# Kernel optimization log

Measured on AMD Instinct MI355X. Metric: run time of the kernel, lower is better.

Reference implementation:

```python
import jax, jax.numpy as jnp
import numpy as np

N_NODES = 100_000
N_EDGES = 1_600_000
F_IN = 32
F_OUT = 32
DIM = 2
K = 5                      # kernel_size per dim (open spline)
KTOT = K ** DIM            # 25 kernel weight matrices
S = 2 ** DIM               # 4 nonzero linear-B-spline basis terms per edge
NEG_SLOPE = 0.2

# offsets over the 2^DIM corners of the spline cell, [S, DIM]
_OFFSETS = np.array([[(s >> d) & 1 for d in range(DIM)] for s in range(S)], dtype=np.int32)
_STRIDES = np.array([K ** d for d in range(DIM)], dtype=np.int32)


def _spline_basis(pseudo):
    """Degree-1 open B-spline basis. pseudo: [E, DIM] in [0,1].
    Returns basis [E, S] and kernel-weight indices widx [E, S]."""
    offsets = jnp.asarray(_OFFSETS)
    strides = jnp.asarray(_STRIDES)
    p = pseudo * (K - 1)                         # open spline scaling
    fl = jnp.floor(p)
    frac = p - fl                                # [E, DIM]
    b = jnp.where(offsets[None] == 0, 1.0 - frac[:, None, :], frac[:, None, :])
    basis = jnp.prod(b, axis=-1)                 # [E, S]
    idx = jnp.clip(fl.astype(jnp.int32)[:, None, :] + offsets[None], 0, K - 1)
    widx = jnp.sum(idx * strides, axis=-1)       # [E, S] in [0, KTOT)
    return basis, widx


def setup_inputs() -> dict:
    key = jax.random.key(0)
    ks = jax.random.split(key, 7)
    x = jax.random.normal(ks[0], (N_NODES, F_IN), dtype=jnp.float32)
    edge_index = jax.random.randint(ks[1], (2, N_EDGES), 0, N_NODES)
    pseudo = jax.random.uniform(ks[2], (N_EDGES, DIM), dtype=jnp.float32)
    bound = 1.0 / np.sqrt(KTOT * F_IN)           # matches reset_parameters uniform(size, ...)
    weight = jax.random.uniform(ks[3], (KTOT, F_IN, F_OUT), jnp.float32, -bound, bound)
    root_weight = jax.random.uniform(ks[4], (F_IN, F_OUT), jnp.float32, -bound, bound)
    att_weight = jax.random.uniform(ks[5], (2 * F_OUT,), jnp.float32, -bound, bound)
    bias = jax.random.uniform(ks[6], (F_OUT,), jnp.float32, -bound, bound)
    return {"x": x, "edge_index": edge_index, "pseudo": pseudo, "weight": weight,
            "root_weight": root_weight, "att_weight": att_weight, "bias": bias}


def reference(x, edge_index, pseudo, weight, root_weight, att_weight, bias):
    row, col = edge_index[0], edge_index[1]      # row = target, col = source
    basis, widx = _spline_basis(pseudo)          # [E,S], [E,S]

    # Precompute x @ W_k for every kernel weight: [N, KTOT, F_OUT]
    xw = jnp.einsum('nf,kfo->nko', x, weight)
    flat = col[:, None] * KTOT + widx            # [E, S] flat (node, kernel) index
    gathered = xw.reshape(-1, F_OUT)[flat]       # [E, S, F_OUT]
    msg = jnp.einsum('es,esf->ef', basis, gathered)  # spline-weighted edge messages

    x_root = x @ root_weight                     # [N, F_OUT]

    # GAT-style attention logits: cat([x_root[row], msg]) . att_weight
    alpha = x_root[row] @ att_weight[:F_OUT] + msg @ att_weight[F_OUT:]
    alpha = jnp.where(alpha > 0, alpha, NEG_SLOPE * alpha)  # leaky relu

    # segment softmax over incoming edges of each target node
    amax = jax.ops.segment_max(alpha, row, num_segments=N_NODES)
    amax = jnp.where(jnp.isfinite(amax), amax, 0.0)
    ex = jnp.exp(alpha - amax[row])
    denom = jax.ops.segment_sum(ex, row, num_segments=N_NODES)
    att = ex / (denom[row] + 1e-16)

    out = jax.ops.segment_sum(msg * att[:, None], row, num_segments=N_NODES)
    return out + x_root + bias
```

## Files before the change

### kernel.cpp

```cpp
#include <hip/hip_runtime.h>
#include <stdint.h>

#define N_NODES 100000
#define N_EDGES 1600000
#define NBLK_SCAN 391

typedef __attribute__((ext_vector_type(8))) short short8;
typedef __attribute__((ext_vector_type(4))) float float4v;

__device__ __forceinline__ unsigned short f32_to_bf16(float f) {
  uint32_t u = __float_as_uint(f);
  u += 0x7fffu + ((u >> 16) & 1u);
  return (unsigned short)(u >> 16);
}
__device__ __forceinline__ float bf16_to_f32(unsigned short h) {
  return __uint_as_float(((uint32_t)h) << 16);
}

__global__ __launch_bounds__(256) void k_zero(
    const float* __restrict__ weight, const float* __restrict__ root_w,
    int* __restrict__ deg, unsigned short* __restrict__ wbf) {
  int tid = threadIdx.x;
  int b = blockIdx.x;
  int i = b * 256 + tid;
  if (i < N_NODES) deg[i] = 0;
  if (b < 100) {
    int e = i;
    int t = e >> 9, rem = e & 511;
    int q = rem >> 7, row = (rem >> 3) & 15, j = rem & 7;
    int km = t >> 1, fin = q * 8 + j, fo = (t & 1) * 16 + row;
    wbf[e] = f32_to_bf16(weight[(km * 32 + fin) * 32 + fo]);
  } else if (b == 100) {
    for (int idx = tid; idx < 1024; idx += 256) {
      int t = 50 + (idx >> 9), rem = idx & 511;
      int q = rem >> 7, row = (rem >> 3) & 15, j = rem & 7;
      int fin = q * 8 + j, fo = (t - 50) * 16 + row;
      wbf[t * 512 + rem] = f32_to_bf16(root_w[fin * 32 + fo]);
    }
  }
}

__global__ __launch_bounds__(256) void k1_xw(
    const float* __restrict__ x, const unsigned short* __restrict__ wbf,
    const int* __restrict__ ei, const float* __restrict__ att_w,
    const float* __restrict__ bias,
    int* __restrict__ deg, unsigned short* __restrict__ rank,
    unsigned short* __restrict__ xw, float* __restrict__ out,
    uint2* __restrict__ od) {
  __shared__ __align__(16) uint2 st[3200];
  int tid = threadIdx.x;
  int b = blockIdx.x;

  int e = b * 256 + tid;
  int rk = atomicAdd(&deg[ei[e]], 1);

  int wave = tid >> 6, lane = tid & 63;
  int quad = lane >> 4, c16 = lane & 15;
  int n0 = b * 16;
  int node = n0 + c16;
  const float* xp = x + (size_t)node * 32 + quad * 8;
  float4 a0 = *reinterpret_cast<const float4*>(xp);
  float4 a1 = *reinterpret_cast<const float4*>(xp + 4);
  short8 af;
  af[0] = (short)f32_to_bf16(a0.x); af[1] = (short)f32_to_bf16(a0.y);
  af[2] = (short)f32_to_bf16(a0.z); af[3] = (short)f32_to_bf16(a0.w);
  af[4] = (short)f32_to_bf16(a1.x); af[5] = (short)f32_to_bf16(a1.y);
  af[6] = (short)f32_to_bf16(a1.z); af[7] = (short)f32_to_bf16(a1.w);

  float rsum = 0.f;
  for (int idx = 0; idx < 13; idx++) {
    int t = wave * 13 + idx;
    short8 bf = *reinterpret_cast<const short8*>(wbf + ((t * 4 + quad) * 16 + c16) * 8);
    float4v acc = {0.f, 0.f, 0.f, 0.f};
    acc = __builtin_amdgcn_mfma_f32_16x16x32_bf16(bf, af, acc, 0, 0, 0);
    if (t < 50) {
      uint2 pk;
      pk.x = (unsigned int)f32_to_bf16(acc[0]) |
             ((unsigned int)f32_to_bf16(acc[1]) << 16);
      pk.y = (unsigned int)f32_to_bf16(acc[2]) |
             ((unsigned int)f32_to_bf16(acc[3]) << 16);
      int tq = t * 4 + quad;
      st[tq * 16 + (c16 ^ (tq & 15))] = pk;
    } else {
      int gfo = (t - 50) * 16 + quad * 4;
      float4 bi = *reinterpret_cast<const float4*>(bias + gfo);
      float4 o;
      o.x = acc[0] + bi.x; o.y = acc[1] + bi.y;
      o.z = acc[2] + bi.z; o.w = acc[3] + bi.w;
      *reinterpret_cast<float4*>(out + (size_t)node * 32 + gfo) = o;
      float4 aw = *reinterpret_cast<const float4*>(att_w + gfo);
      rsum += acc[0] * aw.x + acc[1] * aw.y + acc[2] * aw.z + acc[3] * aw.w;
    }
  }
  if (wave == 3) {
    rsum += __shfl_xor(rsum, 16);
    rsum += __shfl_xor(rsum, 32);
    if (lane < 16) od[node].y = __float_as_uint(rsum);
  }
  __syncthreads();
  uint2* dst = reinterpret_cast<uint2*>(xw) + (size_t)n0 * 200;
  for (int j = tid; j < 3200; j += 256) {
    int nd = j / 200;
    int tq = j - nd * 200;
    dst[j] = st[tq * 16 + (nd ^ (tq & 15))];
  }
  rank[e] = (unsigned short)rk;
}

__global__ __launch_bounds__(256) void kscan1(const int* __restrict__ deg,
                                              int* __restrict__ incl,
                                              int* __restrict__ bsum) {
  __shared__ int s[256];
  int tid = threadIdx.x;
  int i = blockIdx.x * 256 + tid;
  int v = (i < N_NODES) ? deg[i] : 0;
  s[tid] = v;
  __syncthreads();
  for (int d = 1; d < 256; d <<= 1) {
    int t = (tid >= d) ? s[tid - d] : 0;
    __syncthreads();
    s[tid] += t;
    __syncthreads();
  }
  if (i < N_NODES) incl[i] = s[tid];
  if (tid == 255) bsum[blockIdx.x] = s[255];
}

__global__ __launch_bounds__(512) void kscan2(const int* __restrict__ bsum,
                                              int* __restrict__ bbase) {
  __shared__ int s[512];
  int tid = threadIdx.x;
  int v = (tid < NBLK_SCAN) ? bsum[tid] : 0;
  s[tid] = v;
  __syncthreads();
  for (int d = 1; d < 512; d <<= 1) {
    int t = (tid >= d) ? s[tid - d] : 0;
    __syncthreads();
    s[tid] += t;
    __syncthreads();
  }
  if (tid < NBLK_SCAN) bbase[tid] = s[tid] - v;
}

__global__ __launch_bounds__(256) void kscan3(const int* __restrict__ deg,
                                              int* __restrict__ offs,
                                              const int* __restrict__ bbase,
                                              uint2* __restrict__ od) {
  int i = blockIdx.x * 256 + threadIdx.x;
  if (i < N_NODES) {
    int v = offs[i] - deg[i] + bbase[i >> 8];
    offs[i] = v;
    od[i].x = (unsigned int)v;
  }
  if (i == 0) {
    offs[N_NODES] = N_EDGES;
    od[N_NODES].x = (unsigned int)N_EDGES;
  }
}

__global__ __launch_bounds__(256) void kscatter(
    const int* __restrict__ ei, const float* __restrict__ pseudo,
    const uint2* __restrict__ od, const unsigned short* __restrict__ rank,
    uint2* __restrict__ epack) {
  int e = blockIdx.x * 256 + threadIdx.x;
  int r = ei[e];
  int c = ei[N_EDGES + e];
  float p0 = pseudo[2 * e] * 4.f;
  float p1 = pseudo[2 * e + 1] * 4.f;
  int rk = rank[e];
  unsigned int offr = od[r].x;
  float fl0 = floorf(p0), fl1 = floorf(p1);
  float fr0 = p0 - fl0, fr1 = p1 - fl1;
  int i0 = (int)fl0, i1 = (int)fl1;
  int w0 = i0 + 5 * i1;
  int w2 = w0 + 5;
  unsigned int q0 = (unsigned int)(fr0 * 65535.f + 0.5f);
  unsigned int q1 = (unsigned int)(fr1 * 65535.f + 0.5f);
  uint2 pk;
  pk.x = (unsigned int)c | ((unsigned int)w0 << 17) | ((unsigned int)w2 << 22);
  pk.y = q0 | (q1 << 16);
  epack[offr + rk] = pk;
}

__global__ __launch_bounds__(256) void k2_csr(
    const uint2* __restrict__ od, const uint2* __restrict__ epack,
    const unsigned short* __restrict__ xw, const float* __restrict__ att_w,
    float* __restrict__ out) {
  int tid = threadIdx.x;
  int wave = tid >> 6, lane = tid & 63;
  int node = blockIdx.x * 4 + wave;
  if (node >= N_NODES) return;
  int f = lane & 31, half = lane >> 5;
  uint2 v0 = od[node];
  int s0 = (int)v0.x;
  int s1 = (int)od[node + 1].x;
  float rd = __uint_as_float(v0.y);
  float a2 = att_w[32 + f];
  const unsigned short* xwf = xw + f;
  float acc = 0.f, den = 0.f;
  int i = s0 + half;
  const float Q = 1.f / 65535.f;

  for (; i + 6 < s1; i += 8) {
    uint2 p[4];
    p[0] = epack[i];     p[1] = epack[i + 2];
    p[2] = epack[i + 4]; p[3] = epack[i + 6];
    int col[4], o0[4], o2[4];
    float fr0[4], fr1[4];
#pragma unroll
    for (int u = 0; u < 4; u++) {
      col[u] = (int)(p[u].x & 0x1FFFF);
      o0[u] = (int)((p[u].x >> 17) & 31) * 32;
      o2[u] = (int)((p[u].x >> 22) & 31) * 32;
      fr0[u] = (float)(p[u].y & 0xffff) * Q;
      fr1[u] = (float)(p[u].y >> 16) * Q;
    }
    float g0[4], g1[4], g2[4], g3[4];
#pragma unroll
    for (int u = 0; u < 4; u++) {
      const unsigned short* base = xwf + (size_t)col[u] * 800;
      g0[u] = bf16_to_f32(base[o0[u]]);
      g1[u] = bf16_to_f32(base[o0[u] + 32]);
      g2[u] = bf16_to_f32(base[o2[u]]);
      g3[u] = bf16_to_f32(base[o2[u] + 32]);
    }
    float msg[4], t[4];
#pragma unroll
    for (int u = 0; u < 4; u++) {
      float c0 = 1.f - fr0[u], c1 = 1.f - fr1[u];
      msg[u] = c1 * (c0 * g0[u] + fr0[u] * g1[u]) +
               fr1[u] * (c0 * g2[u] + fr0[u] * g3[u]);
      t[u] = msg[u] * a2;
    }
#pragma unroll
    for (int m = 16; m >= 1; m >>= 1) {
      t[0] += __shfl_xor(t[0], m);
      t[1] += __shfl_xor(t[1], m);
      t[2] += __shfl_xor(t[2], m);
      t[3] += __shfl_xor(t[3], m);
    }
#pragma unroll
    for (int u = 0; u < 4; u++) {
      float alpha = rd + t[u];
      alpha = alpha > 0.f ? alpha : 0.2f * alpha;
      float ex = __expf(alpha);
      acc += msg[u] * ex;
      den += ex;
    }
  }
  for (; i < s1; i += 2) {
    uint2 pv = epack[i];
    int col = (int)(pv.x & 0x1FFFF);
    int o0 = (int)((pv.x >> 17) & 31) * 32;
    int o2 = (int)((pv.x >> 22) & 31) * 32;
    float fr0 = (float)(pv.y & 0xffff) * Q;
    float fr1 = (float)(pv.y >> 16) * Q;
    const unsigned short* base = xwf + (size_t)col * 800;
    float g0 = bf16_to_f32(base[o0]);
    float g1 = bf16_to_f32(base[o0 + 32]);
    float g2 = bf16_to_f32(base[o2]);
    float g3 = bf16_to_f32(base[o2 + 32]);
    float c0 = 1.f - fr0, c1 = 1.f - fr1;
    float msg = c1 * (c0 * g0 + fr0 * g1) + fr1 * (c0 * g2 + fr0 * g3);
    float t = msg * a2;
#pragma unroll
    for (int m = 16; m >= 1; m >>= 1) t += __shfl_xor(t, m);
    float alpha = rd + t;
    alpha = alpha > 0.f ? alpha : 0.2f * alpha;
    float ex = __expf(alpha);
    acc += msg * ex;
    den += ex;
  }

  acc += __shfl_xor(acc, 32);
  den += __shfl_xor(den, 32);
  if (half == 0) out[node * 32 + f] += acc / (den + 1e-16f);
}

extern "C" void kernel_launch(void* const* d_in, const int* in_sizes, int n_in,
                              void* d_out, int out_size, void* d_ws, size_t ws_size,
                              hipStream_t stream) {
  const float* x      = (const float*)d_in[0];
  const int*   ei     = (const int*)d_in[1];
  const float* pseudo = (const float*)d_in[2];
  const float* weight = (const float*)d_in[3];
  const float* root_w = (const float*)d_in[4];
  const float* att_w  = (const float*)d_in[5];
  const float* bias   = (const float*)d_in[6];
  float* out = (float*)d_out;

  char* ws = (char*)d_ws;
  unsigned short* xw   = (unsigned short*)ws;
  uint2* od            = (uint2*)(ws + 160000000);
  unsigned short* wbf  = (unsigned short*)(ws + 160800016);
  int* deg             = (int*)(ws + 160853264);
  int* offs            = (int*)(ws + 161253264);
  int* bsum            = (int*)(ws + 161653280);
  int* bbase           = (int*)(ws + 161654880);
  unsigned short* rank = (unsigned short*)(ws + 161656480);
  uint2* epack         = (uint2*)(ws + 164856480);

  hipLaunchKernelGGL(k_zero, dim3(NBLK_SCAN), dim3(256), 0, stream,
                     weight, root_w, deg, wbf);
  hipLaunchKernelGGL(k1_xw, dim3(6250), dim3(256), 0, stream,
                     x, wbf, ei, att_w, bias, deg, rank, xw, out, od);
  hipLaunchKernelGGL(kscan1, dim3(NBLK_SCAN), dim3(256), 0, stream, deg, offs, bsum);
  hipLaunchKernelGGL(kscan2, dim3(1), dim3(512), 0, stream, bsum, bbase);
  hipLaunchKernelGGL(kscan3, dim3(NBLK_SCAN), dim3(256), 0, stream, deg, offs, bbase, od);
  hipLaunchKernelGGL(kscatter, dim3(6250), dim3(256), 0, stream,
                     ei, pseudo, od, rank, epack);
  hipLaunchKernelGGL(k2_csr, dim3(25000), dim3(256), 0, stream,
                     od, epack, xw, att_w, out);
}
```

Before: 333.0 us.

## Replace rank array with atomic cursor scatter and precompute xw offsets

The per-edge rank from the degree-count atomic is no longer stored. The CSR scatter now takes its slot with an atomicAdd on a per-node cursor that the scan initialises. The packed edge word now holds the full xw element offset (col*800 + w0*32), so the aggregation kernel does no bit unpacking and uses fixed strides for the four corner loads. The xw tile store uses nontemporal stores. Edge order within a row becomes nondeterministic, which changes floating-point summation order, and the scatter now pays for a second round of atomics.

```diff
diff --git a/kernel.cpp b/kernel.cpp
--- a/kernel.cpp
+++ b/kernel.cpp
@@ -44,7 +44,7 @@
     const float* __restrict__ x, const unsigned short* __restrict__ wbf,
     const int* __restrict__ ei, const float* __restrict__ att_w,
     const float* __restrict__ bias,
-    int* __restrict__ deg, unsigned short* __restrict__ rank,
+    int* __restrict__ deg,
     unsigned short* __restrict__ xw, float* __restrict__ out,
     uint2* __restrict__ od) {
   __shared__ __align__(16) uint2 st[3200];
@@ -52,7 +52,7 @@
   int b = blockIdx.x;
 
   int e = b * 256 + tid;
-  int rk = atomicAdd(&deg[ei[e]], 1);
+  atomicAdd(&deg[ei[e]], 1);
 
   int wave = tid >> 6, lane = tid & 63;
   int quad = lane >> 4, c16 = lane & 15;
@@ -98,13 +98,15 @@
     if (lane < 16) od[node].y = __float_as_uint(rsum);
   }
   __syncthreads();
-  uint2* dst = reinterpret_cast<uint2*>(xw) + (size_t)n0 * 200;
+  unsigned long long* dst =
+      reinterpret_cast<unsigned long long*>(xw) + (size_t)n0 * 200;
+  const unsigned long long* stq =
+      reinterpret_cast<const unsigned long long*>(st);
   for (int j = tid; j < 3200; j += 256) {
     int nd = j / 200;
     int tq = j - nd * 200;
-    dst[j] = st[tq * 16 + (nd ^ (tq & 15))];
-  }
-  rank[e] = (unsigned short)rk;
+    __builtin_nontemporal_store(stq[tq * 16 + (nd ^ (tq & 15))], dst + j);
+  }
 }
 
 __global__ __launch_bounds__(256) void kscan1(const int* __restrict__ deg,
@@ -143,43 +145,38 @@
 }
 
 __global__ __launch_bounds__(256) void kscan3(const int* __restrict__ deg,
-                                              int* __restrict__ offs,
+                                              const int* __restrict__ incl,
                                               const int* __restrict__ bbase,
-                                              uint2* __restrict__ od) {
+                                              uint2* __restrict__ od,
+                                              int* __restrict__ cur) {
   int i = blockIdx.x * 256 + threadIdx.x;
   if (i < N_NODES) {
-    int v = offs[i] - deg[i] + bbase[i >> 8];
-    offs[i] = v;
+    int v = incl[i] - deg[i] + bbase[i >> 8];
     od[i].x = (unsigned int)v;
-  }
-  if (i == 0) {
-    offs[N_NODES] = N_EDGES;
-    od[N_NODES].x = (unsigned int)N_EDGES;
-  }
+    cur[i] = v;
+  }
+  if (i == 0) od[N_NODES].x = (unsigned int)N_EDGES;
 }
 
 __global__ __launch_bounds__(256) void kscatter(
     const int* __restrict__ ei, const float* __restrict__ pseudo,
-    const uint2* __restrict__ od, const unsigned short* __restrict__ rank,
-    uint2* __restrict__ epack) {
+    int* __restrict__ cur, uint2* __restrict__ epack) {
   int e = blockIdx.x * 256 + threadIdx.x;
   int r = ei[e];
   int c = ei[N_EDGES + e];
   float p0 = pseudo[2 * e] * 4.f;
   float p1 = pseudo[2 * e + 1] * 4.f;
-  int rk = rank[e];
-  unsigned int offr = od[r].x;
   float fl0 = floorf(p0), fl1 = floorf(p1);
   float fr0 = p0 - fl0, fr1 = p1 - fl1;
   int i0 = (int)fl0, i1 = (int)fl1;
   int w0 = i0 + 5 * i1;
-  int w2 = w0 + 5;
   unsigned int q0 = (unsigned int)(fr0 * 65535.f + 0.5f);
   unsigned int q1 = (unsigned int)(fr1 * 65535.f + 0.5f);
+  int pos = atomicAdd(&cur[r], 1);
   uint2 pk;
-  pk.x = (unsigned int)c | ((unsigned int)w0 << 17) | ((unsigned int)w2 << 22);
+  pk.x = (unsigned int)(c * 800 + w0 * 32);
   pk.y = q0 | (q1 << 16);
-  epack[offr + rk] = pk;
+  epack[pos] = pk;
 }
 
 __global__ __launch_bounds__(256) void k2_csr(
@@ -205,24 +202,20 @@
     uint2 p[4];
     p[0] = epack[i];     p[1] = epack[i + 2];
     p[2] = epack[i + 4]; p[3] = epack[i + 6];
-    int col[4], o0[4], o2[4];
     float fr0[4], fr1[4];
 #pragma unroll
     for (int u = 0; u < 4; u++) {
-      col[u] = (int)(p[u].x & 0x1FFFF);
-      o0[u] = (int)((p[u].x >> 17) & 31) * 32;
-      o2[u] = (int)((p[u].x >> 22) & 31) * 32;
       fr0[u] = (float)(p[u].y & 0xffff) * Q;
       fr1[u] = (float)(p[u].y >> 16) * Q;
     }
     float g0[4], g1[4], g2[4], g3[4];
 #pragma unroll
     for (int u = 0; u < 4; u++) {
-      const unsigned short* base = xwf + (size_t)col[u] * 800;
-      g0[u] = bf16_to_f32(base[o0[u]]);
-      g1[u] = bf16_to_f32(base[o0[u] + 32]);
-      g2[u] = bf16_to_f32(base[o2[u]]);
-      g3[u] = bf16_to_f32(base[o2[u] + 32]);
+      const unsigned short* base = xwf + p[u].x;
+      g0[u] = bf16_to_f32(base[0]);
+      g1[u] = bf16_to_f32(base[32]);
+      g2[u] = bf16_to_f32(base[160]);
+      g3[u] = bf16_to_f32(base[192]);
     }
     float msg[4], t[4];
 #pragma unroll
@@ -250,16 +243,13 @@
   }
   for (; i < s1; i += 2) {
     uint2 pv = epack[i];
-    int col = (int)(pv.x & 0x1FFFF);
-    int o0 = (int)((pv.x >> 17) & 31) * 32;
-    int o2 = (int)((pv.x >> 22) & 31) * 32;
     float fr0 = (float)(pv.y & 0xffff) * Q;
     float fr1 = (float)(pv.y >> 16) * Q;
-    const unsigned short* base = xwf + (size_t)col * 800;
-    float g0 = bf16_to_f32(base[o0]);
-    float g1 = bf16_to_f32(base[o0 + 32]);
-    float g2 = bf16_to_f32(base[o2]);
-    float g3 = bf16_to_f32(base[o2 + 32]);
+    const unsigned short* base = xwf + pv.x;
+    float g0 = bf16_to_f32(base[0]);
+    float g1 = bf16_to_f32(base[32]);
+    float g2 = bf16_to_f32(base[160]);
+    float g3 = bf16_to_f32(base[192]);
     float c0 = 1.f - fr0, c1 = 1.f - fr1;
     float msg = c1 * (c0 * g0 + fr0 * g1) + fr1 * (c0 * g2 + fr0 * g3);
     float t = msg * a2;
@@ -294,21 +284,22 @@
   uint2* od            = (uint2*)(ws + 160000000);
   unsigned short* wbf  = (unsigned short*)(ws + 160800016);
   int* deg             = (int*)(ws + 160853264);
-  int* offs            = (int*)(ws + 161253264);
-  int* bsum            = (int*)(ws + 161653280);
-  int* bbase           = (int*)(ws + 161654880);
-  unsigned short* rank = (unsigned short*)(ws + 161656480);
-  uint2* epack         = (uint2*)(ws + 164856480);
+  int* incl            = (int*)(ws + 161253264);
+  int* cur             = (int*)(ws + 161653264);
+  int* bsum            = (int*)(ws + 162053264);
+  int* bbase           = (int*)(ws + 162054864);
+  uint2* epack         = (uint2*)(ws + 162056464);
 
   hipLaunchKernelGGL(k_zero, dim3(NBLK_SCAN), dim3(256), 0, stream,
                      weight, root_w, deg, wbf);
   hipLaunchKernelGGL(k1_xw, dim3(6250), dim3(256), 0, stream,
-                     x, wbf, ei, att_w, bias, deg, rank, xw, out, od);
-  hipLaunchKernelGGL(kscan1, dim3(NBLK_SCAN), dim3(256), 0, stream, deg, offs, bsum);
+                     x, wbf, ei, att_w, bias, deg, xw, out, od);
+  hipLaunchKernelGGL(kscan1, dim3(NBLK_SCAN), dim3(256), 0, stream, deg, incl, bsum);
   hipLaunchKernelGGL(kscan2, dim3(1), dim3(512), 0, stream, bsum, bbase);
-  hipLaunchKernelGGL(kscan3, dim3(NBLK_SCAN), dim3(256), 0, stream, deg, offs, bbase, od);
+  hipLaunchKernelGGL(kscan3, dim3(NBLK_SCAN), dim3(256), 0, stream,
+                     deg, incl, bbase, od, cur);
   hipLaunchKernelGGL(kscatter, dim3(6250), dim3(256), 0, stream,
-                     ei, pseudo, od, rank, epack);
+                     ei, pseudo, cur, epack);
   hipLaunchKernelGGL(k2_csr, dim3(25000), dim3(256), 0, stream,
                      od, epack, xw, att_w, out);
 }
```

Measured after the change: 377.0 us. +13.2%, slower.
